# Kernel tuning notes

Hardware: AMD Instinct MI355X
Metric: run time of the kernel (lower is better)

## Reference

```python
import jax, jax.numpy as jnp
import numpy as np

T, B, D, H = 1024, 8, 1024, 16
NH = D // H  # 64, per-head width (nhid)
W_SCALE = 0.02


def setup_inputs() -> dict:
    key = jax.random.key(0)
    ks = jax.random.split(key, 10)
    return {
        "input_tensor": jax.random.normal(ks[0], (T, B, D), jnp.float32),
        "keys_vector": jax.random.normal(ks[1], (T, B, D), jnp.float32),
        "values_vector": jax.random.normal(ks[2], (T, B, D), jnp.float32),
        # per-head projection weights: [H, D, NH]
        "Wq": jax.random.normal(ks[3], (H, D, NH), jnp.float32) * W_SCALE,
        "bq": jnp.zeros((H, NH), jnp.float32),
        "Wk": jax.random.normal(ks[4], (H, D, NH), jnp.float32) * W_SCALE,
        "bk": jnp.zeros((H, NH), jnp.float32),
        "Wv": jax.random.normal(ks[5], (H, D, NH), jnp.float32) * W_SCALE,
        "bv": jnp.zeros((H, NH), jnp.float32),
        # output projection after concatenating heads
        "Wo": jax.random.normal(ks[6], (D, D), jnp.float32) * W_SCALE,
        "bo": jnp.zeros((D,), jnp.float32),
        "mask": 1,  # True: causal (growing key slice per timestep)
    }


def reference(input_tensor, keys_vector, values_vector, Wq, bq, Wk, bk, Wv, bv, Wo, bo, mask):
    # Vectorized equivalent of the per-timestep loop: query at step t attends
    # to keys/values[:t+1] when mask is set, else to the full sequence.
    q = jnp.einsum('tbd,hdk->tbhk', input_tensor, Wq) + bq   # [T,B,H,NH]
    k = jnp.einsum('sbd,hdk->sbhk', keys_vector, Wk) + bk    # [T,B,H,NH]
    v = jnp.einsum('sbd,hdk->sbhk', values_vector, Wv) + bv  # [T,B,H,NH]

    scale = 1.0 / jnp.sqrt(jnp.float32(NH))
    scores = jnp.einsum('tbhk,sbhk->bhts', q, k) * scale     # [B,H,T,T]
    if mask:
        causal = jnp.tril(jnp.ones((T, T), dtype=bool))      # s <= t
        scores = jnp.where(causal[None, None], scores, jnp.float32(-1e9))
    attn = jax.nn.softmax(scores, axis=-1)                   # over key dim s

    out = jnp.einsum('bhts,sbhk->tbhk', attn, v)             # [T,B,H,NH]
    out = out.reshape(T, B, D)                               # concat heads
    return out @ Wo.T + bo                                   # [T,B,D]
```

## Files before the change

### kernel.cpp

```cpp
#include <hip/hip_runtime.h>

typedef short bf16x8 __attribute__((ext_vector_type(8)));
typedef float f32x4 __attribute__((ext_vector_type(4)));
typedef float f32x16 __attribute__((ext_vector_type(16)));

typedef const __attribute__((address_space(1))) void* gptr_t;
typedef __attribute__((address_space(3))) void* sptr_t;

#define Z16 {0.f,0.f,0.f,0.f,0.f,0.f,0.f,0.f,0.f,0.f,0.f,0.f,0.f,0.f,0.f,0.f}
#define VMCNT(n) asm volatile("s_waitcnt vmcnt(" #n ")" ::: "memory")
#define LGKM0 asm volatile("s_waitcnt lgkmcnt(0)" ::: "memory")
#define SCHEDB __builtin_amdgcn_sched_barrier(0)
#define SBAR __builtin_amdgcn_s_barrier()

__device__ __forceinline__ void glds16(const void* g, void* s) {
  __builtin_amdgcn_global_load_lds((gptr_t)g, (sptr_t)s, 16, 0, 0);
}

__device__ __forceinline__ unsigned short f2bf(float x) {
  unsigned u = __float_as_uint(x);
  u = u + 0x7fffu + ((u >> 16) & 1u);
  return (unsigned short)(u >> 16);
}

__device__ __forceinline__ unsigned packbf(float lo, float hi) {
  return (unsigned)f2bf(lo) | (((unsigned)f2bf(hi)) << 16);
}

__global__ void cvtall(const float* __restrict__ X, const float* __restrict__ KY,
                       const float* __restrict__ VY, const float* __restrict__ Wo,
                       unsigned short* __restrict__ XB, unsigned short* __restrict__ WOB) {
  int stride = gridDim.x * blockDim.x;
  for (int i = blockIdx.x * blockDim.x + threadIdx.x; i < 6553600; i += stride) {
    const float* in; unsigned short* out; int k;
    if (i < 2097152)      { in = X;  out = XB;            k = i; }
    else if (i < 4194304) { in = KY; out = XB + 8388608;  k = i - 2097152; }
    else if (i < 6291456) { in = VY; out = XB + 16777216; k = i - 4194304; }
    else                  { in = Wo; out = WOB;           k = i - 6291456; }
    float4 v = ((const float4*)in)[k];
    uint2 r;
    r.x = packbf(v.x, v.y);
    r.y = packbf(v.z, v.w);
    ((uint2*)out)[k] = r;
  }
}

__global__ __launch_bounds__(256) void wtrans(const float* __restrict__ Wq,
                                              const float* __restrict__ Wk,
                                              const float* __restrict__ Wv,
                                              unsigned short* __restrict__ WT) {
  int m = blockIdx.y >> 4, h = blockIdx.y & 15, d0 = blockIdx.x * 64;
  const float* src = (m == 0 ? Wq : (m == 1 ? Wk : Wv)) + (size_t)h * 65536;
  __shared__ float tile[64][65];
  int c = (threadIdx.x & 15) * 4, r0 = threadIdx.x >> 4;
#pragma unroll
  for (int rr = 0; rr < 4; ++rr) {
    int dr = rr * 16 + r0;
    float4 v = *(const float4*)(src + (size_t)(d0 + dr) * 64 + c);
    tile[dr][c + 0] = v.x; tile[dr][c + 1] = v.y;
    tile[dr][c + 2] = v.z; tile[dr][c + 3] = v.w;
  }
  __syncthreads();
#pragma unroll
  for (int rr = 0; rr < 4; ++rr) {
    int kr = rr * 16 + r0;
    uint2 pk;
    pk.x = packbf(tile[c + 0][kr], tile[c + 1][kr]);
    pk.y = packbf(tile[c + 2][kr], tile[c + 3][kr]);
    *(uint2*)(WT + ((size_t)(m * 1024 + h * 64 + kr)) * 1024 + d0 + c) = pk;
  }
}

template <int MODE>
__global__ __launch_bounds__(512, 2) void gemm256(const unsigned short* __restrict__ Ab,
                                                  const unsigned short* __restrict__ Bb,
                                                  const float* __restrict__ bi0,
                                                  const float* __restrict__ bi1,
                                                  const float* __restrict__ bi2,
                                                  void* __restrict__ outp) {
  extern __shared__ __align__(16) char lds[];
  const int K = 1024;
  int z = blockIdx.z;
  const unsigned short* A = Ab + (size_t)z * 8192 * 1024;
  const unsigned short* BT = Bb + (size_t)z * 1024 * 1024;
  const float* bias = (MODE == 0) ? (z == 0 ? bi0 : (z == 1 ? bi1 : bi2)) : bi0;
  int m0 = blockIdx.x * 256, n0 = blockIdx.y * 256;
  int tid = threadIdx.x, wid = tid >> 6, l = tid & 63, ml = l & 15, hi = l >> 4;
  int wr = (wid >> 2) * 128, wc = (wid & 3) * 64;
  int srow = l >> 3;
  int ksw = ((l & 7) << 4) ^ (srow << 4);
  f32x4 acc[8][4] = {};
#pragma unroll
  for (int i = 0; i < 4; ++i) {
    int rb = (wid * 4 + i) * 8 + srow;
    glds16((const char*)(A + (size_t)(m0 + rb) * K) + ksw, lds + (wid * 4 + i) * 1024);
    glds16((const char*)(BT + (size_t)(n0 + rb) * K) + ksw, lds + 32768 + (wid * 4 + i) * 1024);
  }
  int cur = 0;
  for (int kt = 0; kt < 16; ++kt) {
    if (kt < 15) {
      char* nb = lds + (cur ^ 1) * 65536;
      int ko = (kt + 1) * 64;
#pragma unroll
      for (int i = 0; i < 4; ++i) {
        int rb = (wid * 4 + i) * 8 + srow;
        glds16((const char*)(A + (size_t)(m0 + rb) * K + ko) + ksw, nb + (wid * 4 + i) * 1024);
        glds16((const char*)(BT + (size_t)(n0 + rb) * K + ko) + ksw, nb + 32768 + (wid * 4 + i) * 1024);
      }
      VMCNT(8);
    } else {
      VMCNT(0);
    }
    SCHEDB; SBAR; SCHEDB;
    char* As = lds + cur * 65536;
    char* Bs = As + 32768;
#pragma unroll
    for (int ks = 0; ks < 2; ++ks) {
      bf16x8 af[8], bfr[4];
#pragma unroll
      for (int mf = 0; mf < 8; ++mf) {
        int row = wr + mf * 16 + ml;
        af[mf] = *(const bf16x8*)(As + row * 128 + ((ks * 64 + (hi << 4)) ^ ((row & 7) << 4)));
      }
#pragma unroll
      for (int nf = 0; nf < 4; ++nf) {
        int row = wc + nf * 16 + ml;
        bfr[nf] = *(const bf16x8*)(Bs + row * 128 + ((ks * 64 + (hi << 4)) ^ ((row & 7) << 4)));
      }
      __builtin_amdgcn_s_setprio(1);
#pragma unroll
      for (int mf = 0; mf < 8; ++mf)
#pragma unroll
        for (int nf = 0; nf < 4; ++nf)
          acc[mf][nf] = __builtin_amdgcn_mfma_f32_16x16x32_bf16(af[mf], bfr[nf], acc[mf][nf], 0, 0, 0);
      __builtin_amdgcn_s_setprio(0);
    }
    SCHEDB; LGKM0; SBAR;
    cur ^= 1;
  }
  if (MODE == 1) {
#pragma unroll
    for (int pass = 0; pass < 2; ++pass) {
      if ((wid >> 2) == pass) {
#pragma unroll
        for (int nf = 0; nf < 4; ++nf) {
          int col = wc + nf * 16 + ml;
          float bv = bias[n0 + col];
#pragma unroll
          for (int mf = 0; mf < 8; ++mf)
#pragma unroll
            for (int r = 0; r < 4; ++r) {
              int row = mf * 16 + (hi << 2) + r;
              int byte = col * 4;
              *(float*)(lds + row * 1024 + ((byte & ~15) ^ ((row & 7) << 4)) + (byte & 15)) =
                  acc[mf][nf][r] + bv;
            }
        }
      }
      __syncthreads();
      int rr = tid >> 2, q = tid & 3;
      float* drow = (float*)outp + (size_t)(m0 + pass * 128 + rr) * 1024 + n0 + q * 64;
#pragma unroll
      for (int j = 0; j < 16; ++j) {
        uint4 d = *(uint4*)(lds + rr * 1024 + ((q * 256 + j * 16) ^ ((rr & 7) << 4)));
        *(uint4*)(drow + j * 4) = d;
      }
      __syncthreads();
    }
    return;
  }
#pragma unroll
  for (int nf = 0; nf < 4; ++nf) {
    int col = wc + nf * 16 + ml;
    float bv = bias[n0 + col];
#pragma unroll
    for (int mf = 0; mf < 8; ++mf)
#pragma unroll
      for (int r = 0; r < 4; ++r) {
        int row = wr + mf * 16 + (hi << 2) + r;
        float v = acc[mf][nf][r] + bv;
        float pv = __shfl_xor(v, 1);
        unsigned pk = (ml & 1) ? packbf(pv, v) : packbf(v, pv);
        *(unsigned*)(lds + row * 512 + (((col * 2) & ~3) ^ ((row & 7) << 4))) = pk;
      }
  }
  __syncthreads();
  unsigned short* ob = (unsigned short*)outp + (size_t)z * 8388608;
  if (z != 2) {
#pragma unroll
    for (int q = 0; q < 2; ++q) {
      int id = q * 512 + tid;
      int rr = id >> 2, hh = id & 3;
      int t = (m0 + rr) >> 3, b = (m0 + rr) & 7;
      int h = (n0 >> 6) + hh;
      unsigned short* dst = ob + (size_t)(b * 16 + h) * 65536 + (size_t)t * 64;
#pragma unroll
      for (int j = 0; j < 8; ++j) {
        uint4 d = *(uint4*)(lds + rr * 512 + ((hh * 128 + j * 16) ^ ((rr & 7) << 4)));
        *(uint4*)(dst + j * 8) = d;
      }
    }
  } else {
    int t0 = m0 >> 3;
#pragma unroll
    for (int q = 0; q < 4; ++q) {
      int id = q * 512 + tid;
      int k = id & 63;
      int bh2 = id >> 6;
      int b = bh2 >> 2, hh = bh2 & 3;
      int colb = (hh * 64 + k) * 2;
      union { unsigned short u[32]; uint4 v[4]; } tmp;
#pragma unroll
      for (int tp = 0; tp < 32; ++tp)
        tmp.u[tp] = *(unsigned short*)(lds + (tp * 8 + b) * 512 + (colb ^ (b << 4)));
      int h = (n0 >> 6) + hh;
      unsigned short* dst = ob + (size_t)(b * 16 + h) * 65536 + (size_t)k * 1024 + t0;
#pragma unroll
      for (int j = 0; j < 4; ++j) *(uint4*)(dst + j * 8) = tmp.v[j];
    }
  }
}

__global__ __launch_bounds__(512, 4) void attn_k(const unsigned short* __restrict__ Qp,
                                                 const unsigned short* __restrict__ Kp,
                                                 const unsigned short* __restrict__ VTp,
                                                 unsigned short* __restrict__ Op,
                                                 const int* __restrict__ maskp) {
  int lin = blockIdx.x;
  int xcd = lin & 7, idx = lin >> 3;
  int bh = xcd + 8 * (idx >> 2);
  int j = idx & 3;
  const size_t base = (size_t)bh * 65536;
  int tid = threadIdx.x, w = tid >> 6, l = tid & 63;
  int ml5 = l & 31, hi1 = l >> 5;
  int half = w & 1, pi = w >> 1;
  int stripe = (pi == 0) ? j : (pi == 1) ? (15 - j) : (pi == 2) ? (7 - j) : (8 + j);
  int tw0 = stripe * 64 + half * 32;
  int t_glob = tw0 + ml5;
  __shared__ __align__(16) char lds[32768];
  int msk = *maskp;
  const float CE = 0.18033688011112042f;
  bf16x8 bq[4];
#pragma unroll
  for (int kd = 0; kd < 4; ++kd)
    bq[kd] = *(const bf16x8*)(Qp + base + (size_t)t_glob * 64 + kd * 16 + hi1 * 8);
  f32x16 o0 = Z16, o1 = Z16;
  float m_run = -3e38f, l_run = 0.f;
  int nt = msk ? (16 - j) : 16;
  int diag = stripe;
  int srow = l >> 3, kphys = (l & 7) << 4;
  int row = w * 8 + srow;
  int klog = kphys ^ (srow << 4);
  int swz = (ml5 & 7) << 4;
  glds16((const char*)(Kp + base + (size_t)row * 64) + klog, lds + w * 1024);
  glds16((const char*)(VTp + base + (size_t)row * 1024) + klog, lds + 8192 + w * 1024);
  int cur = 0;
  for (int st = 0; st < nt; ++st) {
    if (st + 1 < nt) {
      char* nb = lds + (cur ^ 1) * 16384;
      glds16((const char*)(Kp + base + (size_t)((st + 1) * 64 + row) * 64) + klog, nb + w * 1024);
      glds16((const char*)(VTp + base + (size_t)row * 1024 + (st + 1) * 64) + klog, nb + 8192 + w * 1024);
      VMCNT(4);
    } else {
      VMCNT(0);
    }
    SCHEDB; SBAR; SCHEDB;
    if (!msk || st <= diag) {
      char* Ks = lds + cur * 16384;
      char* Vs = Ks + 8192;
      f32x16 s0 = Z16, s1 = Z16;
      __builtin_amdgcn_s_setprio(1);
#pragma unroll
      for (int kd = 0; kd < 4; ++kd) {
        int koff = kd * 32 + hi1 * 16;
        bf16x8 a0 = *(const bf16x8*)(Ks + ml5 * 128 + (koff ^ swz));
        bf16x8 a1 = *(const bf16x8*)(Ks + (32 + ml5) * 128 + (koff ^ swz));
        s0 = __builtin_amdgcn_mfma_f32_32x32x16_bf16(a0, bq[kd], s0, 0, 0, 0);
        s1 = __builtin_amdgcn_mfma_f32_32x32x16_bf16(a1, bq[kd], s1, 0, 0, 0);
      }
      __builtin_amdgcn_s_setprio(0);
      if (msk && st == diag) {
#pragma unroll
        for (int r = 0; r < 16; ++r) {
          int sl = st * 64 + (r & 3) + 8 * (r >> 2) + 4 * hi1;
          if (sl > t_glob) s0[r] = -1e30f;
          if (sl + 32 > t_glob) s1[r] = -1e30f;
        }
      }
      float t8[8];
#pragma unroll
      for (int r = 0; r < 8; ++r)
        t8[r] = fmaxf(fmaxf(s0[r], s0[r + 8]), fmaxf(s1[r], s1[r + 8]));
      float tm = fmaxf(fmaxf(fmaxf(t8[0], t8[1]), fmaxf(t8[2], t8[3])),
                       fmaxf(fmaxf(t8[4], t8[5]), fmaxf(t8[6], t8[7])));
      tm = fmaxf(tm, __shfl_xor(tm, 32));
      float m_old = m_run;
      float m_new = fmaxf(m_old, tm);
      m_run = m_new;
      float sc2 = exp2f((m_old - m_new) * CE);
      float mC = m_new * CE;
#pragma unroll
      for (int r = 0; r < 16; ++r) {
        s0[r] = exp2f(fmaf(s0[r], CE, -mC));
        s1[r] = exp2f(fmaf(s1[r], CE, -mC));
      }
      float a8[8];
#pragma unroll
      for (int r = 0; r < 8; ++r)
        a8[r] = (s0[r] + s0[r + 8]) + (s1[r] + s1[r + 8]);
      float ps = ((a8[0] + a8[1]) + (a8[2] + a8[3])) + ((a8[4] + a8[5]) + (a8[6] + a8[7]));
      ps += __shfl_xor(ps, 32);
      l_run = l_run * sc2 + ps;
#pragma unroll
      for (int r = 0; r < 16; ++r) { o0[r] *= sc2; o1[r] *= sc2; }
      unsigned cc0[4][2], cc1[4][2];
#pragma unroll
      for (int q = 0; q < 4; ++q) {
        cc0[q][0] = packbf(s0[4 * q + 0], s0[4 * q + 1]);
        cc0[q][1] = packbf(s0[4 * q + 2], s0[4 * q + 3]);
        cc1[q][0] = packbf(s1[4 * q + 0], s1[4 * q + 1]);
        cc1[q][1] = packbf(s1[4 * q + 2], s1[4 * q + 3]);
      }
#define CCa(a, p) ((a) < 4 ? cc0[(a) & 3][p] : cc1[(a) & 3][p])
      union U4 { unsigned u[4]; bf16x8 v; };
      bf16x8 pb[4];
#pragma unroll
      for (int kb = 0; kb < 4; ++kb) {
        U4 t;
#pragma unroll
        for (int p = 0; p < 2; ++p) {
          unsigned x = CCa(2 * kb, p), y = CCa(2 * kb + 1, p);
          unsigned v = hi1 ? x : y;
          unsigned wv = hi1 ? y : x;
          unsigned vs = __shfl_xor(v, 32);
          t.u[p]     = hi1 ? vs : wv;
          t.u[2 + p] = hi1 ? wv : vs;
        }
        pb[kb] = t.v;
      }
#undef CCa
      __builtin_amdgcn_s_setprio(1);
#pragma unroll
      for (int kb = 0; kb < 4; ++kb) {
        int koff = kb * 32 + hi1 * 16;
        bf16x8 v0 = *(const bf16x8*)(Vs + ml5 * 128 + (koff ^ swz));
        bf16x8 v1 = *(const bf16x8*)(Vs + (32 + ml5) * 128 + (koff ^ swz));
        o0 = __builtin_amdgcn_mfma_f32_32x32x16_bf16(v0, pb[kb], o0, 0, 0, 0);
        o1 = __builtin_amdgcn_mfma_f32_32x32x16_bf16(v1, pb[kb], o1, 0, 0, 0);
      }
      __builtin_amdgcn_s_setprio(0);
    }
    SCHEDB; LGKM0; SBAR;
    cur ^= 1;
  }
  float rl = 1.0f / l_run;
  int b = bh >> 4, h = bh & 15;
  unsigned short* orow = Op + (size_t)(t_glob * 8 + b) * 1024 + h * 64;
#pragma unroll
  for (int q2 = 0; q2 < 4; ++q2) {
    uint2 pk0, pk1;
    pk0.x = packbf(o0[4 * q2 + 0] * rl, o0[4 * q2 + 1] * rl);
    pk0.y = packbf(o0[4 * q2 + 2] * rl, o0[4 * q2 + 3] * rl);
    *(uint2*)(orow + 4 * hi1 + 8 * q2) = pk0;
    pk1.x = packbf(o1[4 * q2 + 0] * rl, o1[4 * q2 + 1] * rl);
    pk1.y = packbf(o1[4 * q2 + 2] * rl, o1[4 * q2 + 3] * rl);
    *(uint2*)(orow + 32 + 4 * hi1 + 8 * q2) = pk1;
  }
}

extern "C" void kernel_launch(void* const* d_in, const int* in_sizes, int n_in,
                              void* d_out, int out_size, void* d_ws, size_t ws_size,
                              hipStream_t stream) {
  const float* X  = (const float*)d_in[0];
  const float* KY = (const float*)d_in[1];
  const float* VY = (const float*)d_in[2];
  const float* Wq = (const float*)d_in[3];
  const float* bq = (const float*)d_in[4];
  const float* Wk = (const float*)d_in[5];
  const float* bk = (const float*)d_in[6];
  const float* Wv = (const float*)d_in[7];
  const float* bv = (const float*)d_in[8];
  const float* Wo = (const float*)d_in[9];
  const float* bo = (const float*)d_in[10];
  const int* mask = (const int*)d_in[11];
  char* ws = (char*)d_ws;
  unsigned short* XB  = (unsigned short*)(ws);
  unsigned short* WT  = (unsigned short*)(ws + 48ll * 1024 * 1024);
  unsigned short* WOB = (unsigned short*)(ws + 54ll * 1024 * 1024);
  unsigned short* QP  = (unsigned short*)(ws + 56ll * 1024 * 1024);
  unsigned short* OP  = (unsigned short*)(ws + 104ll * 1024 * 1024);

  cvtall<<<2048, 256, 0, stream>>>(X, KY, VY, Wo, XB, WOB);
  wtrans<<<dim3(16, 48), 256, 0, stream>>>(Wq, Wk, Wv, WT);
  gemm256<0><<<dim3(32, 4, 3), 512, 131072, stream>>>(XB, WT, bq, bk, bv, QP);
  attn_k<<<512, 512, 0, stream>>>(QP, QP + 8388608, QP + 16777216, OP, mask);
  gemm256<1><<<dim3(32, 4, 1), 512, 131072, stream>>>(OP, WOB, bo, bo, bo, d_out);
}
```

Baseline: 228.5 us.

## Retile GEMMs to 256x128 with 32x32 MFMA and triple-buffered LDS pipeline

```diff
diff --git a/kernel.cpp b/kernel.cpp
--- a/kernel.cpp
+++ b/kernel.cpp
@@ -84,135 +84,134 @@
   const unsigned short* A = Ab + (size_t)z * 8192 * 1024;
   const unsigned short* BT = Bb + (size_t)z * 1024 * 1024;
   const float* bias = (MODE == 0) ? (z == 0 ? bi0 : (z == 1 ? bi1 : bi2)) : bi0;
-  int m0 = blockIdx.x * 256, n0 = blockIdx.y * 256;
-  int tid = threadIdx.x, wid = tid >> 6, l = tid & 63, ml = l & 15, hi = l >> 4;
-  int wr = (wid >> 2) * 128, wc = (wid & 3) * 64;
+  int m0 = blockIdx.x * 256, n0 = blockIdx.y * 128;
+  int tid = threadIdx.x, wid = tid >> 6, l = tid & 63;
+  int ml5 = l & 31, hi1 = l >> 5;
+  int wr = (wid & 3) * 64, wc = (wid >> 2) * 64;
   int srow = l >> 3;
-  int ksw = ((l & 7) << 4) ^ (srow << 4);
-  f32x4 acc[8][4] = {};
-#pragma unroll
-  for (int i = 0; i < 4; ++i) {
-    int rb = (wid * 4 + i) * 8 + srow;
-    glds16((const char*)(A + (size_t)(m0 + rb) * K) + ksw, lds + (wid * 4 + i) * 1024);
-    glds16((const char*)(BT + (size_t)(n0 + rb) * K) + ksw, lds + 32768 + (wid * 4 + i) * 1024);
-  }
-  int cur = 0;
-  for (int kt = 0; kt < 16; ++kt) {
-    if (kt < 15) {
-      char* nb = lds + (cur ^ 1) * 65536;
-      int ko = (kt + 1) * 64;
+  int ksw = ((l & 7) << 4) ^ ((srow & 7) << 4);
+  f32x16 acc[2][2] = {};
+#pragma unroll
+  for (int t0 = 0; t0 < 2; ++t0) {
+    char* nb = lds + t0 * 49152;
+    int ko = t0 * 64;
+#pragma unroll
+    for (int i = 0; i < 4; ++i) {
+      int c = wid * 4 + i;
+      glds16((const char*)(A + (size_t)(m0 + c * 8 + srow) * K + ko) + ksw, nb + c * 1024);
+    }
+#pragma unroll
+    for (int i = 0; i < 2; ++i) {
+      int c2 = wid * 2 + i;
+      glds16((const char*)(BT + (size_t)(n0 + c2 * 8 + srow) * K + ko) + ksw, nb + 32768 + c2 * 1024);
+    }
+  }
+  int bsel = 0;
+  for (int t = 0; t < 16; ++t) {
+    SCHEDB; LGKM0;
+    if (t < 15) { VMCNT(6); } else { VMCNT(0); }
+    SBAR; SCHEDB;
+    if (t + 2 < 16) {
+      int b2 = bsel + 2; if (b2 >= 3) b2 -= 3;
+      char* nb = lds + b2 * 49152;
+      int ko = (t + 2) * 64;
 #pragma unroll
       for (int i = 0; i < 4; ++i) {
-        int rb = (wid * 4 + i) * 8 + srow;
-        glds16((const char*)(A + (size_t)(m0 + rb) * K + ko) + ksw, nb + (wid * 4 + i) * 1024);
-        glds16((const char*)(BT + (size_t)(n0 + rb) * K + ko) + ksw, nb + 32768 + (wid * 4 + i) * 1024);
-      }
-      VMCNT(8);
-    } else {
-      VMCNT(0);
-    }
-    SCHEDB; SBAR; SCHEDB;
-    char* As = lds + cur * 65536;
+        int c = wid * 4 + i;
+        glds16((const char*)(A + (size_t)(m0 + c * 8 + srow) * K + ko) + ksw, nb + c * 1024);
+      }
+#pragma unroll
+      for (int i = 0; i < 2; ++i) {
+        int c2 = wid * 2 + i;
+        glds16((const char*)(BT + (size_t)(n0 + c2 * 8 + srow) * K + ko) + ksw, nb + 32768 + c2 * 1024);
+      }
+    }
+    char* As = lds + bsel * 49152;
     char* Bs = As + 32768;
 #pragma unroll
-    for (int ks = 0; ks < 2; ++ks) {
-      bf16x8 af[8], bfr[4];
-#pragma unroll
-      for (int mf = 0; mf < 8; ++mf) {
-        int row = wr + mf * 16 + ml;
-        af[mf] = *(const bf16x8*)(As + row * 128 + ((ks * 64 + (hi << 4)) ^ ((row & 7) << 4)));
-      }
-#pragma unroll
-      for (int nf = 0; nf < 4; ++nf) {
-        int row = wc + nf * 16 + ml;
-        bfr[nf] = *(const bf16x8*)(Bs + row * 128 + ((ks * 64 + (hi << 4)) ^ ((row & 7) << 4)));
-      }
+    for (int ks = 0; ks < 4; ++ks) {
+      int koff = ks * 32 + hi1 * 16;
+      int ra0 = wr + ml5, ra1 = wr + 32 + ml5;
+      int rb0 = wc + ml5, rb1 = wc + 32 + ml5;
+      bf16x8 a0 = *(const bf16x8*)(As + ra0 * 128 + (koff ^ ((ra0 & 7) << 4)));
+      bf16x8 a1 = *(const bf16x8*)(As + ra1 * 128 + (koff ^ ((ra1 & 7) << 4)));
+      bf16x8 b0 = *(const bf16x8*)(Bs + rb0 * 128 + (koff ^ ((rb0 & 7) << 4)));
+      bf16x8 b1 = *(const bf16x8*)(Bs + rb1 * 128 + (koff ^ ((rb1 & 7) << 4)));
       __builtin_amdgcn_s_setprio(1);
-#pragma unroll
-      for (int mf = 0; mf < 8; ++mf)
-#pragma unroll
-        for (int nf = 0; nf < 4; ++nf)
-          acc[mf][nf] = __builtin_amdgcn_mfma_f32_16x16x32_bf16(af[mf], bfr[nf], acc[mf][nf], 0, 0, 0);
+      acc[0][0] = __builtin_amdgcn_mfma_f32_32x32x16_bf16(a0, b0, acc[0][0], 0, 0, 0);
+      acc[0][1] = __builtin_amdgcn_mfma_f32_32x32x16_bf16(a0, b1, acc[0][1], 0, 0, 0);
+      acc[1][0] = __builtin_amdgcn_mfma_f32_32x32x16_bf16(a1, b0, acc[1][0], 0, 0, 0);
+      acc[1][1] = __builtin_amdgcn_mfma_f32_32x32x16_bf16(a1, b1, acc[1][1], 0, 0, 0);
       __builtin_amdgcn_s_setprio(0);
     }
-    SCHEDB; LGKM0; SBAR;
-    cur ^= 1;
-  }
+    bsel += 1; if (bsel >= 3) bsel = 0;
+  }
+  __syncthreads();
   if (MODE == 1) {
 #pragma unroll
-    for (int pass = 0; pass < 2; ++pass) {
-      if ((wid >> 2) == pass) {
-#pragma unroll
-        for (int nf = 0; nf < 4; ++nf) {
-          int col = wc + nf * 16 + ml;
-          float bv = bias[n0 + col];
-#pragma unroll
-          for (int mf = 0; mf < 8; ++mf)
-#pragma unroll
-            for (int r = 0; r < 4; ++r) {
-              int row = mf * 16 + (hi << 2) + r;
-              int byte = col * 4;
-              *(float*)(lds + row * 1024 + ((byte & ~15) ^ ((row & 7) << 4)) + (byte & 15)) =
-                  acc[mf][nf][r] + bv;
-            }
+    for (int nf = 0; nf < 2; ++nf) {
+      int col = wc + nf * 32 + ml5;
+      float bv = bias[n0 + col];
+#pragma unroll
+      for (int mf = 0; mf < 2; ++mf)
+#pragma unroll
+        for (int r = 0; r < 16; ++r) {
+          int row = wr + mf * 32 + (r & 3) + 8 * (r >> 2) + 4 * hi1;
+          int byte = col * 4;
+          *(float*)(lds + row * 512 + ((byte & ~15) ^ ((row & 7) << 4)) + (byte & 15)) =
+              acc[mf][nf][r] + bv;
         }
-      }
-      __syncthreads();
-      int rr = tid >> 2, q = tid & 3;
-      float* drow = (float*)outp + (size_t)(m0 + pass * 128 + rr) * 1024 + n0 + q * 64;
-#pragma unroll
-      for (int j = 0; j < 16; ++j) {
-        uint4 d = *(uint4*)(lds + rr * 1024 + ((q * 256 + j * 16) ^ ((rr & 7) << 4)));
-        *(uint4*)(drow + j * 4) = d;
-      }
-      __syncthreads();
+    }
+    __syncthreads();
+    int rr = tid >> 1, q = tid & 1;
+    float* drow = (float*)outp + (size_t)(m0 + rr) * 1024 + n0 + q * 64;
+#pragma unroll
+    for (int j = 0; j < 16; ++j) {
+      uint4 d = *(uint4*)(lds + rr * 512 + ((q * 256 + j * 16) ^ ((rr & 7) << 4)));
+      *(uint4*)(drow + j * 4) = d;
     }
     return;
   }
 #pragma unroll
-  for (int nf = 0; nf < 4; ++nf) {
-    int col = wc + nf * 16 + ml;
+  for (int nf = 0; nf < 2; ++nf) {
+    int col = wc + nf * 32 + ml5;
     float bv = bias[n0 + col];
 #pragma unroll
-    for (int mf = 0; mf < 8; ++mf)
-#pragma unroll
-      for (int r = 0; r < 4; ++r) {
-        int row = wr + mf * 16 + (hi << 2) + r;
+    for (int mf = 0; mf < 2; ++mf)
+#pragma unroll
+      for (int r = 0; r < 16; ++r) {
+        int row = wr + mf * 32 + (r & 3) + 8 * (r >> 2) + 4 * hi1;
         float v = acc[mf][nf][r] + bv;
         float pv = __shfl_xor(v, 1);
-        unsigned pk = (ml & 1) ? packbf(pv, v) : packbf(v, pv);
-        *(unsigned*)(lds + row * 512 + (((col * 2) & ~3) ^ ((row & 7) << 4))) = pk;
+        unsigned pk = (ml5 & 1) ? packbf(pv, v) : packbf(v, pv);
+        *(unsigned*)(lds + row * 256 + (((col * 2) & ~3) ^ ((row & 7) << 4))) = pk;
       }
   }
   __syncthreads();
   unsigned short* ob = (unsigned short*)outp + (size_t)z * 8388608;
   if (z != 2) {
-#pragma unroll
-    for (int q = 0; q < 2; ++q) {
-      int id = q * 512 + tid;
-      int rr = id >> 2, hh = id & 3;
-      int t = (m0 + rr) >> 3, b = (m0 + rr) & 7;
-      int h = (n0 >> 6) + hh;
-      unsigned short* dst = ob + (size_t)(b * 16 + h) * 65536 + (size_t)t * 64;
-#pragma unroll
-      for (int j = 0; j < 8; ++j) {
-        uint4 d = *(uint4*)(lds + rr * 512 + ((hh * 128 + j * 16) ^ ((rr & 7) << 4)));
-        *(uint4*)(dst + j * 8) = d;
-      }
+    int rr = tid >> 1, hh = tid & 1;
+    int t = (m0 + rr) >> 3, b = (m0 + rr) & 7;
+    int h = (n0 >> 6) + hh;
+    unsigned short* dst = ob + (size_t)(b * 16 + h) * 65536 + (size_t)t * 64;
+#pragma unroll
+    for (int j = 0; j < 8; ++j) {
+      uint4 d = *(uint4*)(lds + rr * 256 + ((hh * 128 + j * 16) ^ ((rr & 7) << 4)));
+      *(uint4*)(dst + j * 8) = d;
     }
   } else {
     int t0 = m0 >> 3;
 #pragma unroll
-    for (int q = 0; q < 4; ++q) {
+    for (int q = 0; q < 2; ++q) {
       int id = q * 512 + tid;
       int k = id & 63;
       int bh2 = id >> 6;
-      int b = bh2 >> 2, hh = bh2 & 3;
+      int b = bh2 >> 1, hh = bh2 & 1;
       int colb = (hh * 64 + k) * 2;
       union { unsigned short u[32]; uint4 v[4]; } tmp;
 #pragma unroll
       for (int tp = 0; tp < 32; ++tp)
-        tmp.u[tp] = *(unsigned short*)(lds + (tp * 8 + b) * 512 + (colb ^ (b << 4)));
+        tmp.u[tp] = *(unsigned short*)(lds + (tp * 8 + b) * 256 + (colb ^ (b << 4)));
       int h = (n0 >> 6) + hh;
       unsigned short* dst = ob + (size_t)(b * 16 + h) * 65536 + (size_t)k * 1024 + t0;
 #pragma unroll
@@ -392,7 +391,7 @@
 
   cvtall<<<2048, 256, 0, stream>>>(X, KY, VY, Wo, XB, WOB);
   wtrans<<<dim3(16, 48), 256, 0, stream>>>(Wq, Wk, Wv, WT);
-  gemm256<0><<<dim3(32, 4, 3), 512, 131072, stream>>>(XB, WT, bq, bk, bv, QP);
+  gemm256<0><<<dim3(32, 8, 3), 512, 147456, stream>>>(XB, WT, bq, bk, bv, QP);
   attn_k<<<512, 512, 0, stream>>>(QP, QP + 8388608, QP + 16777216, OP, mask);
-  gemm256<1><<<dim3(32, 4, 1), 512, 131072, stream>>>(OP, WOB, bo, bo, bo, d_out);
-}
+  gemm256<1><<<dim3(32, 8, 1), 512, 147456, stream>>>(OP, WOB, bo, bo, bo, d_out);
+}
```

After: 210.2 us. 8.0% less time.

## Split GEMM k-tile into four quadrant MFMA phases interleaved with staged prefetch

Applied to the files above, without the earlier changes.

```diff
diff --git a/kernel.cpp b/kernel.cpp
--- a/kernel.cpp
+++ b/kernel.cpp
@@ -88,74 +88,130 @@
   int tid = threadIdx.x, wid = tid >> 6, l = tid & 63, ml = l & 15, hi = l >> 4;
   int wr = (wid >> 2) * 128, wc = (wid & 3) * 64;
   int srow = l >> 3;
-  int ksw = ((l & 7) << 4) ^ (srow << 4);
+  int ksw = ((l & 7) << 4) ^ ((srow & 7) << 4);
   f32x4 acc[8][4] = {};
 #pragma unroll
   for (int i = 0; i < 4; ++i) {
-    int rb = (wid * 4 + i) * 8 + srow;
-    glds16((const char*)(A + (size_t)(m0 + rb) * K) + ksw, lds + (wid * 4 + i) * 1024);
-    glds16((const char*)(BT + (size_t)(n0 + rb) * K) + ksw, lds + 32768 + (wid * 4 + i) * 1024);
-  }
+    int c = wid * 4 + i;
+    glds16((const char*)(A + (size_t)(m0 + c * 8 + srow) * K) + ksw, lds + c * 1024);
+    glds16((const char*)(BT + (size_t)(n0 + c * 8 + srow) * K) + ksw, lds + 32768 + c * 1024);
+  }
+  VMCNT(0); SCHEDB; SBAR;
   int cur = 0;
-  for (int kt = 0; kt < 16; ++kt) {
-    if (kt < 15) {
-      char* nb = lds + (cur ^ 1) * 65536;
-      int ko = (kt + 1) * 64;
-#pragma unroll
-      for (int i = 0; i < 4; ++i) {
-        int rb = (wid * 4 + i) * 8 + srow;
-        glds16((const char*)(A + (size_t)(m0 + rb) * K + ko) + ksw, nb + (wid * 4 + i) * 1024);
-        glds16((const char*)(BT + (size_t)(n0 + rb) * K + ko) + ksw, nb + 32768 + (wid * 4 + i) * 1024);
-      }
-      VMCNT(8);
-    } else {
-      VMCNT(0);
-    }
-    SCHEDB; SBAR; SCHEDB;
+  for (int t = 0; t < 16; ++t) {
     char* As = lds + cur * 65536;
     char* Bs = As + 32768;
-#pragma unroll
-    for (int ks = 0; ks < 2; ++ks) {
-      bf16x8 af[8], bfr[4];
-#pragma unroll
-      for (int mf = 0; mf < 8; ++mf) {
+    char* nx = lds + (cur ^ 1) * 65536;
+    int ko = (t + 1) * 64;
+    bool st = t < 15;
+    bf16x8 af[4][2], bfr[2][2][2];
+#pragma unroll
+    for (int mf = 0; mf < 4; ++mf)
+#pragma unroll
+      for (int ks = 0; ks < 2; ++ks) {
         int row = wr + mf * 16 + ml;
-        af[mf] = *(const bf16x8*)(As + row * 128 + ((ks * 64 + (hi << 4)) ^ ((row & 7) << 4)));
-      }
-#pragma unroll
-      for (int nf = 0; nf < 4; ++nf) {
+        af[mf][ks] = *(const bf16x8*)(As + row * 128 + ((ks * 64 + (hi << 4)) ^ ((row & 7) << 4)));
+      }
+#pragma unroll
+    for (int nf = 0; nf < 2; ++nf)
+#pragma unroll
+      for (int ks = 0; ks < 2; ++ks) {
         int row = wc + nf * 16 + ml;
-        bfr[nf] = *(const bf16x8*)(Bs + row * 128 + ((ks * 64 + (hi << 4)) ^ ((row & 7) << 4)));
-      }
-      __builtin_amdgcn_s_setprio(1);
-#pragma unroll
-      for (int mf = 0; mf < 8; ++mf)
-#pragma unroll
-        for (int nf = 0; nf < 4; ++nf)
-          acc[mf][nf] = __builtin_amdgcn_mfma_f32_16x16x32_bf16(af[mf], bfr[nf], acc[mf][nf], 0, 0, 0);
-      __builtin_amdgcn_s_setprio(0);
-    }
-    SCHEDB; LGKM0; SBAR;
+        bfr[0][nf][ks] = *(const bf16x8*)(Bs + row * 128 + ((ks * 64 + (hi << 4)) ^ ((row & 7) << 4)));
+      }
+    if (st) {
+#pragma unroll
+      for (int i = 0; i < 4; ++i) {
+        int c = wid * 4 + i;
+        glds16((const char*)(A + (size_t)(m0 + c * 8 + srow) * K + ko) + ksw, nx + c * 1024);
+      }
+    }
+    SCHEDB; SBAR; LGKM0; SCHEDB;
+    __builtin_amdgcn_s_setprio(1);
+#pragma unroll
+    for (int ks = 0; ks < 2; ++ks)
+#pragma unroll
+      for (int mf = 0; mf < 4; ++mf)
+#pragma unroll
+        for (int nf = 0; nf < 2; ++nf)
+          acc[mf][nf] = __builtin_amdgcn_mfma_f32_16x16x32_bf16(af[mf][ks], bfr[0][nf][ks], acc[mf][nf], 0, 0, 0);
+    __builtin_amdgcn_s_setprio(0);
+    SCHEDB; SBAR;
+#pragma unroll
+    for (int nf = 0; nf < 2; ++nf)
+#pragma unroll
+      for (int ks = 0; ks < 2; ++ks) {
+        int row = wc + 32 + nf * 16 + ml;
+        bfr[1][nf][ks] = *(const bf16x8*)(Bs + row * 128 + ((ks * 64 + (hi << 4)) ^ ((row & 7) << 4)));
+      }
+    if (st) {
+#pragma unroll
+      for (int i = 0; i < 4; ++i) {
+        int c = wid * 4 + i;
+        glds16((const char*)(BT + (size_t)(n0 + c * 8 + srow) * K + ko) + ksw, nx + 32768 + c * 1024);
+      }
+    }
+    SCHEDB; SBAR; LGKM0; SCHEDB;
+    __builtin_amdgcn_s_setprio(1);
+#pragma unroll
+    for (int ks = 0; ks < 2; ++ks)
+#pragma unroll
+      for (int mf = 0; mf < 4; ++mf)
+#pragma unroll
+        for (int nf = 0; nf < 2; ++nf)
+          acc[mf][2 + nf] = __builtin_amdgcn_mfma_f32_16x16x32_bf16(af[mf][ks], bfr[1][nf][ks], acc[mf][2 + nf], 0, 0, 0);
+    __builtin_amdgcn_s_setprio(0);
+    SCHEDB; SBAR;
+#pragma unroll
+    for (int mf = 0; mf < 4; ++mf)
+#pragma unroll
+      for (int ks = 0; ks < 2; ++ks) {
+        int row = wr + 64 + mf * 16 + ml;
+        af[mf][ks] = *(const bf16x8*)(As + row * 128 + ((ks * 64 + (hi << 4)) ^ ((row & 7) << 4)));
+      }
+    SCHEDB; SBAR; LGKM0; SCHEDB;
+    __builtin_amdgcn_s_setprio(1);
+#pragma unroll
+    for (int ks = 0; ks < 2; ++ks)
+#pragma unroll
+      for (int mf = 0; mf < 4; ++mf)
+#pragma unroll
+        for (int nf = 0; nf < 2; ++nf)
+          acc[4 + mf][2 + nf] = __builtin_amdgcn_mfma_f32_16x16x32_bf16(af[mf][ks], bfr[1][nf][ks], acc[4 + mf][2 + nf], 0, 0, 0);
+    __builtin_amdgcn_s_setprio(0);
+    SCHEDB; SBAR;
+    __builtin_amdgcn_s_setprio(1);
+#pragma unroll
+    for (int ks = 0; ks < 2; ++ks)
+#pragma unroll
+      for (int mf = 0; mf < 4; ++mf)
+#pragma unroll
+        for (int nf = 0; nf < 2; ++nf)
+          acc[4 + mf][nf] = __builtin_amdgcn_mfma_f32_16x16x32_bf16(af[mf][ks], bfr[0][nf][ks], acc[4 + mf][nf], 0, 0, 0);
+    __builtin_amdgcn_s_setprio(0);
+    if (st) { VMCNT(0); }
+    SCHEDB; SBAR;
     cur ^= 1;
   }
+  __syncthreads();
   if (MODE == 1) {
 #pragma unroll
     for (int pass = 0; pass < 2; ++pass) {
       if ((wid >> 2) == pass) {
 #pragma unroll
-        for (int nf = 0; nf < 4; ++nf) {
-          int col = wc + nf * 16 + ml;
-          float bv = bias[n0 + col];
-#pragma unroll
-          for (int mf = 0; mf < 8; ++mf)
+        for (int mfg = 0; mfg < 8; ++mfg)
+#pragma unroll
+          for (int nfg = 0; nfg < 4; ++nfg) {
+            int col = wc + (nfg >> 1) * 32 + (nfg & 1) * 16 + ml;
+            float bv = bias[n0 + col];
 #pragma unroll
             for (int r = 0; r < 4; ++r) {
-              int row = mf * 16 + (hi << 2) + r;
+              int row = (mfg >> 2) * 64 + (mfg & 3) * 16 + (hi << 2) + r;
               int byte = col * 4;
               *(float*)(lds + row * 1024 + ((byte & ~15) ^ ((row & 7) << 4)) + (byte & 15)) =
-                  acc[mf][nf][r] + bv;
+                  acc[mfg][nfg][r] + bv;
             }
-        }
+          }
       }
       __syncthreads();
       int rr = tid >> 2, q = tid & 3;
@@ -170,20 +226,20 @@
     return;
   }
 #pragma unroll
-  for (int nf = 0; nf < 4; ++nf) {
-    int col = wc + nf * 16 + ml;
-    float bv = bias[n0 + col];
-#pragma unroll
-    for (int mf = 0; mf < 8; ++mf)
+  for (int mfg = 0; mfg < 8; ++mfg)
+#pragma unroll
+    for (int nfg = 0; nfg < 4; ++nfg) {
+      int col = wc + (nfg >> 1) * 32 + (nfg & 1) * 16 + ml;
+      float bv = bias[n0 + col];
 #pragma unroll
       for (int r = 0; r < 4; ++r) {
-        int row = wr + mf * 16 + (hi << 2) + r;
-        float v = acc[mf][nf][r] + bv;
+        int row = wr + (mfg >> 2) * 64 + (mfg & 3) * 16 + (hi << 2) + r;
+        float v = acc[mfg][nfg][r] + bv;
         float pv = __shfl_xor(v, 1);
         unsigned pk = (ml & 1) ? packbf(pv, v) : packbf(v, pv);
         *(unsigned*)(lds + row * 512 + (((col * 2) & ~3) ^ ((row & 7) << 4))) = pk;
       }
-  }
+    }
   __syncthreads();
   unsigned short* ob = (unsigned short*)outp + (size_t)z * 8388608;
   if (z != 2) {
```

Result: no change. 225.5 us (-1.3%).
